# Kernel optimization log

Measured on AMD Instinct MI355X. Metric: run time of the kernel, lower is better.

## Reference

```python
import jax, jax.numpy as jnp
import numpy as np
from jax import lax

D = 1024          # channel / embedding dim
K = 2048          # codebook size
BN_EPS = 1e-5


def conv1d(x, w, b, stride):
    # x: [N, C, L], w: [O, I, k]
    y = lax.conv_general_dilated(x, w, window_strides=(stride,), padding='VALID',
                                 dimension_numbers=('NCH', 'OIH', 'NCH'))
    return y + b[None, :, None]


def batchnorm1d(x, gamma, beta):
    # training-mode BN: batch statistics over (N, L) per channel, biased variance
    mean = jnp.mean(x, axis=(0, 2), keepdims=True)
    var = jnp.var(x, axis=(0, 2), keepdims=True)
    return (x - mean) * lax.rsqrt(var + BN_EPS) * gamma[None, :, None] + beta[None, :, None]


def setup_inputs() -> dict:
    key = jax.random.key(0)
    ks = jax.random.split(key, 8)
    x = jax.random.normal(ks[0], (32, D, 1024), dtype=jnp.float32)
    conv1_w = jax.random.normal(ks[1], (D, D, 4), dtype=jnp.float32) * 0.02
    conv1_b = jnp.zeros((D,), dtype=jnp.float32)
    bn1_g = jnp.ones((D,), dtype=jnp.float32)
    bn1_b = jnp.zeros((D,), dtype=jnp.float32)
    conv2_w = jax.random.normal(ks[2], (D, D, 1), dtype=jnp.float32) * 0.02
    conv2_b = jnp.zeros((D,), dtype=jnp.float32)
    bn2_g = jnp.ones((D,), dtype=jnp.float32)
    bn2_b = jnp.zeros((D,), dtype=jnp.float32)
    codebook = jax.random.normal(ks[3], (K, D), dtype=jnp.float32)
    return {'x': x, 'conv1_w': conv1_w, 'conv1_b': conv1_b,
            'bn1_g': bn1_g, 'bn1_b': bn1_b,
            'conv2_w': conv2_w, 'conv2_b': conv2_b,
            'bn2_g': bn2_g, 'bn2_b': bn2_b,
            'codebook': codebook}


def encoder(x, conv1_w, conv1_b, bn1_g, bn1_b, conv2_w, conv2_b, bn2_g, bn2_b):
    h = conv1d(x, conv1_w, conv1_b, stride=2)           # [B, D, L']
    # ResidualWrapper(BN -> ReLU -> Conv1x1)
    r = batchnorm1d(h, bn1_g, bn1_b)
    r = jax.nn.relu(r)
    r = conv1d(r, conv2_w, conv2_b, stride=1)
    h = h + r
    h = batchnorm1d(h, bn2_g, bn2_b)
    return h


def vq(h, codebook):
    # axis=1 -> move channel axis last: [B, L', D]
    z = jnp.moveaxis(h, 1, -1)
    # squared Euclidean distances via ||z||^2 - 2 z.e + ||e||^2  (cdist+argmin)
    z2 = jnp.sum(z * z, axis=-1, keepdims=True)                  # [B, L', 1]
    e2 = jnp.sum(codebook * codebook, axis=-1)                   # [K]
    ze = jnp.einsum('bld,kd->blk', z, codebook)                  # [B, L', K]
    dist2 = z2 - 2.0 * ze + e2[None, None, :]
    ids = jnp.argmin(dist2, axis=-1)                             # [B, L'] int
    q = codebook[ids]                                            # [B, L', D]
    sg = lax.stop_gradient
    commitment = jnp.mean((z - sg(q)) ** 2)
    codebook_loss = jnp.mean((sg(z) - q) ** 2)
    # straight-through estimator
    q_st = z + sg(q - z)
    q_st = jnp.moveaxis(q_st, -1, 1)                             # back to [B, D, L']
    return q_st, ids, commitment, codebook_loss


def reference(x, conv1_w, conv1_b, bn1_g, bn1_b, conv2_w, conv2_b, bn2_g, bn2_b, codebook):
    h = encoder(x, conv1_w, conv1_b, bn1_g, bn1_b, conv2_w, conv2_b, bn2_g, bn2_b)
    q_st, ids, commitment, codebook_loss = vq(h, codebook)
    return q_st, ids, commitment, codebook_loss
```

## Files before the change

kernel.cpp:

```cpp
#include <hip/hip_runtime.h>
#include <hip/hip_bf16.h>
#include <cstdint>

#define DD 1024
#define LIN 1024
#define LP 511
#define LPAD 512
#define NBATCH 32
#define KCB 2048
#define BN_EPS 1e-5f

#define OUT_IDS 16744448u
#define OUT_LOSS 16760800u

#define WS_H1 0
#define WS_UNI 16777216
#define WS_XH  (WS_UNI)
#define WS_XL  (WS_UNI + 16777728)
#define WS_WTH (WS_UNI + 33555456)
#define WS_WTL (WS_UNI + 35652608)
#define WS_T2  (WS_UNI)
#define WS_RH  (WS_UNI + 16777216)
#define WS_RL  (WS_UNI + 25165824)
#define WS_ZH  WS_RH
#define WS_ZL  WS_RL
#define WS_W2H (WS_UNI + 33554432)
#define WS_W2L (WS_UNI + 34078720)
#define WS_CBH (WS_UNI + 34603008)
#define WS_CBL (WS_UNI + 35651584)
#define WS_AUX (WS_UNI + 37749760)
#define WS_A1 (WS_AUX + 0)
#define WS_B1 (WS_AUX + 1024)
#define WS_A2 (WS_AUX + 2048)
#define WS_B2 (WS_AUX + 3072)
#define WS_E2 (WS_AUX + 4096)
#define WS_SLOTS (WS_AUX + 6144)
#define WS_LOSS (WS_AUX + 6144 + 32704)

typedef __attribute__((ext_vector_type(8))) short bf16x8;
typedef __attribute__((ext_vector_type(4))) float f32x4;
typedef __attribute__((ext_vector_type(4))) unsigned short ushort4v;

__device__ __forceinline__ void async_cp16(const void* gsrc, void* ldst) {
  __builtin_amdgcn_global_load_lds(
      (const __attribute__((address_space(1))) unsigned int*)gsrc,
      (__attribute__((address_space(3))) unsigned int*)ldst, 16, 0, 0);
}

__device__ __forceinline__ void bf16split(float v, unsigned short& hi, unsigned short& lo) {
  __hip_bfloat16 h = __float2bfloat16(v);
  float hf = __bfloat162float(h);
  __hip_bfloat16 l = __float2bfloat16(v - hf);
  hi = *(unsigned short*)&h;
  lo = *(unsigned short*)&l;
}

__device__ inline float blockReduce256(float v, float* sb) {
#pragma unroll
  for (int off = 32; off > 0; off >>= 1) v += __shfl_down(v, off);
  __syncthreads();
  if ((threadIdx.x & 63) == 0) sb[threadIdx.x >> 6] = v;
  __syncthreads();
  return sb[0] + sb[1] + sb[2] + sb[3];
}

__device__ __forceinline__ void mfma_tiles_k(
    const unsigned short* __restrict__ srcw, unsigned short* sm, int lane,
    int wid, int nkc, int mrow, int nrow, int ko, f32x4 (&acc)[4][4]) {
  const unsigned short* As = sm;
  const unsigned short* Als = sm + 4096;
  const unsigned short* Bs = sm + 8192;
  const unsigned short* Bls = sm + 12288;
  for (int kc = 0; kc < nkc; ++kc) {
    const unsigned short* lanesrc =
        srcw + (size_t)kc * 32 + (size_t)(lane >> 2) * 1024 + (lane & 3) * 8;
    char* ldsbase = (char*)sm + wid * 8192;
#pragma unroll
    for (int q = 0; q < 8; ++q)
      async_cp16(lanesrc + (size_t)q * 16 * 1024, ldsbase + q * 1024);
    __syncthreads();
    bf16x8 fbh[4], fbl[4];
#pragma unroll
    for (int nt = 0; nt < 4; ++nt) {
      int r = nrow + nt * 16;
      fbh[nt] = *(const bf16x8*)(Bs + r * 32 + ko);
      fbl[nt] = *(const bf16x8*)(Bls + r * 32 + ko);
    }
#pragma unroll
    for (int mt = 0; mt < 4; ++mt) {
      int r = mrow + mt * 16;
      bf16x8 fah = *(const bf16x8*)(As + r * 32 + ko);
      bf16x8 fal = *(const bf16x8*)(Als + r * 32 + ko);
#pragma unroll
      for (int nt = 0; nt < 4; ++nt) {
        acc[mt][nt] = __builtin_amdgcn_mfma_f32_16x16x32_bf16(fah, fbh[nt], acc[mt][nt], 0, 0, 0);
        acc[mt][nt] = __builtin_amdgcn_mfma_f32_16x16x32_bf16(fah, fbl[nt], acc[mt][nt], 0, 0, 0);
        acc[mt][nt] = __builtin_amdgcn_mfma_f32_16x16x32_bf16(fal, fbh[nt], acc[mt][nt], 0, 0, 0);
      }
    }
    __syncthreads();
  }
}

__global__ __launch_bounds__(256) void split_w1_kernel(
    const float* __restrict__ w, unsigned short* __restrict__ wth,
    unsigned short* __restrict__ wtl) {
  int idx = blockIdx.x * 256 + threadIdx.x;
  int o = idx >> 10, i = idx & 1023;
  float4 v = *(const float4*)&w[(size_t)idx * 4];
  float vv[4] = {v.x, v.y, v.z, v.w};
#pragma unroll
  for (int t = 0; t < 4; ++t) {
    unsigned short hi, lo;
    bf16split(vv[t], hi, lo);
    size_t off = (((size_t)(t << 10) + o) << 10) + i;
    wth[off] = hi;
    wtl[off] = lo;
  }
}

__global__ __launch_bounds__(256) void split_rows_kernel(
    const float* __restrict__ src, unsigned short* __restrict__ dsth,
    unsigned short* __restrict__ dstl) {
  size_t base = ((size_t)blockIdx.x * 256 + threadIdx.x) * 4;
  float4 v = *(const float4*)&src[base];
  float vv[4] = {v.x, v.y, v.z, v.w};
  ushort4v h, l;
#pragma unroll
  for (int j = 0; j < 4; ++j) {
    unsigned short hi, lo;
    bf16split(vv[j], hi, lo);
    h[j] = hi;
    l[j] = lo;
  }
  *(ushort4v*)&dsth[base] = h;
  *(ushort4v*)&dstl[base] = l;
}

__global__ __launch_bounds__(256) void split_x_kernel(
    const float* __restrict__ x, unsigned short* __restrict__ xh,
    unsigned short* __restrict__ xl) {
  __shared__ float lsT[128 * 65];
  const int l0 = blockIdx.x * 128;
  const int i0 = blockIdx.y * 64;
  const int nB = blockIdx.z;
  const int tid = threadIdx.x;
#pragma unroll
  for (int p = 0; p < 8; ++p) {
    int flat = p * 256 + tid;
    int row = flat >> 5, col4 = (flat & 31) * 4;
    float4 v = *(const float4*)&x[((size_t)nB * DD + i0 + row) * LIN + l0 + col4];
    lsT[(col4 + 0) * 65 + row] = v.x;
    lsT[(col4 + 1) * 65 + row] = v.y;
    lsT[(col4 + 2) * 65 + row] = v.z;
    lsT[(col4 + 3) * 65 + row] = v.w;
  }
  __syncthreads();
  const int lo2 = (l0 >> 1);
#pragma unroll
  for (int p = 0; p < 16; ++p) {
    int cp = p * 4 + (tid >> 6);
    int il = tid & 63;
    float vE = lsT[(2 * cp) * 65 + il];
    float vO = lsT[(2 * cp + 1) * 65 + il];
    unsigned short hE, lE, hO, lO;
    bf16split(vE, hE, lE);
    bf16split(vO, hO, lO);
    size_t dE = (((size_t)(0 * 32 + nB) * 512) + lo2 + cp) * 1024 + i0 + il;
    size_t dO = (((size_t)(1 * 32 + nB) * 512) + lo2 + cp) * 1024 + i0 + il;
    xh[dE] = hE; xl[dE] = lE;
    xh[dO] = hO; xl[dO] = lO;
  }
}

__global__ __launch_bounds__(256) void trans_affine_split_kernel(
    const float* __restrict__ src, const float* __restrict__ a,
    const float* __restrict__ b, unsigned short* __restrict__ dsth,
    unsigned short* __restrict__ dstl, int do_relu) {
  __shared__ float lsT[128 * 65];
  const int l0 = blockIdx.x * 128;
  const int i0 = blockIdx.y * 64;
  const int nB = blockIdx.z;
  const int tid = threadIdx.x;
#pragma unroll
  for (int p = 0; p < 8; ++p) {
    int flat = p * 256 + tid;
    int row = flat >> 5, col4 = (flat & 31) * 4;
    float4 v = *(const float4*)&src[((size_t)nB * DD + i0 + row) * LPAD + l0 + col4];
    lsT[(col4 + 0) * 65 + row] = v.x;
    lsT[(col4 + 1) * 65 + row] = v.y;
    lsT[(col4 + 2) * 65 + row] = v.z;
    lsT[(col4 + 3) * 65 + row] = v.w;
  }
  __syncthreads();
  const int il = tid & 63;
  const float ac = a[i0 + il], bc = b[i0 + il];
#pragma unroll
  for (int p = 0; p < 32; ++p) {
    int cp = p * 4 + (tid >> 6);
    float v = fmaf(ac, lsT[cp * 65 + il], bc);
    if (do_relu) v = fmaxf(v, 0.f);
    unsigned short hi, lo;
    bf16split(v, hi, lo);
    size_t d = (((size_t)nB * 512) + l0 + cp) * 1024 + i0 + il;
    dsth[d] = hi;
    dstl[d] = lo;
  }
}

__global__ __launch_bounds__(256) void conv1_mfma_kernel(
    const unsigned short* __restrict__ wth, const unsigned short* __restrict__ wtl,
    const unsigned short* __restrict__ xh, const unsigned short* __restrict__ xl,
    const float* __restrict__ bias, float* __restrict__ h1) {
  __shared__ unsigned short sm[16384];
  const int tid = threadIdx.x;
  const int wid = tid >> 6, lane = tid & 63;
  const int lb = blockIdx.x * 128, ob = blockIdx.y * 128, nB = blockIdx.z;

  f32x4 acc[4][4];
#pragma unroll
  for (int a = 0; a < 4; ++a)
#pragma unroll
    for (int b = 0; b < 4; ++b) acc[a][b] = (f32x4){0.f, 0.f, 0.f, 0.f};

  const int wm = wid & 1, wn = wid >> 1;
  const int mrow = (wm << 6) + (lane & 15);
  const int nrow = (wn << 6) + (lane & 15);
  const int ko = (lane >> 4) << 3;

  for (int t = 0; t < 4; ++t) {
    const unsigned short* srcw;
    if (wid == 0)
      srcw = wth + (((size_t)(t << 10) + ob) << 10);
    else if (wid == 1)
      srcw = wtl + (((size_t)(t << 10) + ob) << 10);
    else {
      const unsigned short* xp = (wid == 2) ? xh : xl;
      srcw = xp + ((((size_t)((t & 1) * 32 + nB) * 512) + lb + (t >> 1)) << 10);
    }
    mfma_tiles_k(srcw, sm, lane, wid, 32, mrow, nrow, ko, acc);
  }

#pragma unroll
  for (int mt = 0; mt < 4; ++mt) {
    const int o_base = ob + (wm << 6) + mt * 16 + ((lane >> 4) << 2);
#pragma unroll
    for (int nt = 0; nt < 4; ++nt) {
      const int l = lb + (wn << 6) + nt * 16 + (lane & 15);
      if (l < LP) {
#pragma unroll
        for (int rg = 0; rg < 4; ++rg)
          h1[((size_t)(nB << 10) + o_base + rg) * LPAD + l] =
              acc[mt][nt][rg] + bias[o_base + rg];
      }
    }
  }
}

__global__ __launch_bounds__(256) void conv2_mfma_kernel(
    const unsigned short* __restrict__ w2h, const unsigned short* __restrict__ w2l,
    const unsigned short* __restrict__ rh, const unsigned short* __restrict__ rl,
    const float* __restrict__ b2c, const float* __restrict__ h1,
    float* __restrict__ t2) {
  __shared__ unsigned short sm[16384];
  const int tid = threadIdx.x;
  const int wid = tid >> 6, lane = tid & 63;
  const int lb = blockIdx.x * 128, ob = blockIdx.y * 128, nB = blockIdx.z;

  f32x4 acc[4][4];
#pragma unroll
  for (int a = 0; a < 4; ++a)
#pragma unroll
    for (int b = 0; b < 4; ++b) acc[a][b] = (f32x4){0.f, 0.f, 0.f, 0.f};

  const int wm = wid & 1, wn = wid >> 1;
  const int mrow = (wm << 6) + (lane & 15);
  const int nrow = (wn << 6) + (lane & 15);
  const int ko = (lane >> 4) << 3;

  const unsigned short* srcw =
      (wid == 0) ? w2h + ((size_t)ob << 10)
    : (wid == 1) ? w2l + ((size_t)ob << 10)
    : (wid == 2) ? rh + (((size_t)nB * 512 + lb) << 10)
                 : rl + (((size_t)nB * 512 + lb) << 10);
  mfma_tiles_k(srcw, sm, lane, wid, 32, mrow, nrow, ko, acc);

#pragma unroll
  for (int mt = 0; mt < 4; ++mt) {
    const int o_base = ob + (wm << 6) + mt * 16 + ((lane >> 4) << 2);
#pragma unroll
    for (int nt = 0; nt < 4; ++nt) {
      const int l = lb + (wn << 6) + nt * 16 + (lane & 15);
      if (l < LP) {
#pragma unroll
        for (int rg = 0; rg < 4; ++rg) {
          size_t off = ((size_t)(nB << 10) + o_base + rg) * LPAD + l;
          t2[off] = h1[off] + acc[mt][nt][rg] + b2c[o_base + rg];
        }
      }
    }
  }
}

__global__ __launch_bounds__(256) void dist_mfma_kernel(
    const unsigned short* __restrict__ cbh, const unsigned short* __restrict__ cbl,
    const unsigned short* __restrict__ zh, const unsigned short* __restrict__ zl,
    const float* __restrict__ e2, unsigned long long* __restrict__ slots) {
  __shared__ unsigned short sm[16384];
  __shared__ unsigned long long best[128];
  const int tid = threadIdx.x;
  const int wid = tid >> 6, lane = tid & 63;
  const int lb = blockIdx.x * 128, kb = blockIdx.y * 128, nB = blockIdx.z;

  f32x4 acc[4][4];
#pragma unroll
  for (int a = 0; a < 4; ++a)
#pragma unroll
    for (int b = 0; b < 4; ++b) acc[a][b] = (f32x4){0.f, 0.f, 0.f, 0.f};

  const int wm = wid & 1, wn = wid >> 1;
  const int mrow = (wm << 6) + (lane & 15);
  const int nrow = (wn << 6) + (lane & 15);
  const int ko = (lane >> 4) << 3;

  const unsigned short* srcw =
      (wid == 0) ? cbh + ((size_t)kb << 10)
    : (wid == 1) ? cbl + ((size_t)kb << 10)
    : (wid == 2) ? zh + (((size_t)nB * 512 + lb) << 10)
                 : zl + (((size_t)nB * 512 + lb) << 10);
  mfma_tiles_k(srcw, sm, lane, wid, 32, mrow, nrow, ko, acc);

  if (tid < 128) best[tid] = ~0ULL;
  __syncthreads();
#pragma unroll
  for (int nt = 0; nt < 4; ++nt) {
    const int col = (wn << 6) + nt * 16 + (lane & 15);
    float dmin = 3.4e38f;
    int kmin = 0;
#pragma unroll
    for (int mt = 0; mt < 4; ++mt) {
      const int kbase = kb + (wm << 6) + mt * 16 + ((lane >> 4) << 2);
#pragma unroll
      for (int rg = 0; rg < 4; ++rg) {
        float dist = fmaf(-2.f, acc[mt][nt][rg], e2[kbase + rg]);
        if (dist < dmin) { dmin = dist; kmin = kbase + rg; }
      }
    }
    unsigned long long pk =
        ((unsigned long long)__float_as_uint(dmin) << 32) | (unsigned)kmin;
    atomicMin(&best[col], pk);
  }
  __syncthreads();
  if (tid < 128) {
    int l = lb + tid;
    if (l < LP) atomicMin(&slots[(size_t)nB * LP + l], best[tid]);
  }
}

__global__ __launch_bounds__(256) void bn_stats_kernel(
    const float* __restrict__ src, const float* __restrict__ gamma,
    const float* __restrict__ beta, float* __restrict__ a_out,
    float* __restrict__ b_out) {
  __shared__ float sb[4];
  const int c = blockIdx.x;
  const float* p = src + (size_t)c * LPAD;
  float s1 = 0.f, s2 = 0.f;
  for (int idx = threadIdx.x; idx < NBATCH * LP; idx += 256) {
    int nn = idx / LP;
    int l = idx - nn * LP;
    float v = p[(size_t)nn * DD * LPAD + l];
    s1 += v;
    s2 = fmaf(v, v, s2);
  }
  s1 = blockReduce256(s1, sb);
  s2 = blockReduce256(s2, sb);
  if (threadIdx.x == 0) {
    const float inv = 1.f / (float)(NBATCH * LP);
    float m = s1 * inv;
    float var = fmaf(-m, m, s2 * inv);
    float a = gamma[c] * rsqrtf(var + BN_EPS);
    a_out[c] = a;
    b_out[c] = fmaf(-m, a, beta[c]);
  }
}

__global__ __launch_bounds__(256) void e2_kernel(const float* __restrict__ cb,
                                                 float* __restrict__ e2) {
  __shared__ float sb[4];
  const int k = blockIdx.x;
  float s = 0.f;
  for (int d = threadIdx.x; d < DD; d += 256) {
    float v = cb[(size_t)k * DD + d];
    s = fmaf(v, v, s);
  }
  s = blockReduce256(s, sb);
  if (threadIdx.x == 0) e2[k] = s;
}

__global__ __launch_bounds__(256) void gather_kernel(
    const float* __restrict__ t2, const float* __restrict__ cb,
    const float* __restrict__ a2, const float* __restrict__ b2,
    const unsigned long long* __restrict__ slots, float* __restrict__ out,
    float* __restrict__ loss_acc) {
  __shared__ int ks[64];
  __shared__ float sb[4];
  const int l0 = blockIdx.x * 64;
  const int n = blockIdx.y;
  const int tid = threadIdx.x, tx = tid & 63, ty = tid >> 6;
  if (tid < 64) {
    int l = l0 + tid;
    int k = 0;
    if (l < LP) {
      k = (int)(unsigned)(slots[(size_t)n * LP + l] & 0xffffffffULL);
      out[OUT_IDS + (size_t)n * LP + l] = (float)k;
    }
    ks[tid] = k;
  }
  __syncthreads();
  const int l = l0 + tx;
  const bool valid = (l < LP);
  const int k = ks[tx];
  const float* cbk = cb + (size_t)k * DD;
  const float* tn = t2 + (size_t)n * DD * LPAD;
  float* qo = out + (size_t)n * DD * LP;
  float lsum = 0.f;
  for (int d0 = 0; d0 < DD; d0 += 4) {
    const int d = d0 + ty;
    float q = cbk[d];
    if (valid) {
      float z = fmaf(a2[d], tn[(size_t)d * LPAD + l], b2[d]);
      qo[(size_t)d * LP + l] = q;
      float e = z - q;
      lsum = fmaf(e, e, lsum);
    }
  }
  lsum = blockReduce256(lsum, sb);
  if (tid == 0) atomicAdd(loss_acc, lsum);
}

__global__ void finalize_kernel(const float* __restrict__ loss_acc,
                                float* __restrict__ out) {
  if (threadIdx.x == 0) {
    float m = loss_acc[0] * (1.f / 16744448.f);
    out[OUT_LOSS] = m;
    out[OUT_LOSS + 1] = m;
  }
}

extern "C" void kernel_launch(void* const* d_in, const int* in_sizes, int n_in,
                              void* d_out, int out_size, void* d_ws,
                              size_t ws_size, hipStream_t stream) {
  const float* x = (const float*)d_in[0];
  const float* w1 = (const float*)d_in[1];
  const float* b1c = (const float*)d_in[2];
  const float* g1 = (const float*)d_in[3];
  const float* be1 = (const float*)d_in[4];
  const float* w2 = (const float*)d_in[5];
  const float* b2c = (const float*)d_in[6];
  const float* g2 = (const float*)d_in[7];
  const float* be2 = (const float*)d_in[8];
  const float* cb = (const float*)d_in[9];
  float* out = (float*)d_out;
  float* ws = (float*)d_ws;

  float* h1 = ws + WS_H1;
  float* t2 = ws + WS_T2;
  unsigned short* xh = (unsigned short*)(ws + WS_XH);
  unsigned short* xl = (unsigned short*)(ws + WS_XL);
  unsigned short* wth = (unsigned short*)(ws + WS_WTH);
  unsigned short* wtl = (unsigned short*)(ws + WS_WTL);
  unsigned short* rh = (unsigned short*)(ws + WS_RH);
  unsigned short* rl = (unsigned short*)(ws + WS_RL);
  unsigned short* zh = (unsigned short*)(ws + WS_ZH);
  unsigned short* zl = (unsigned short*)(ws + WS_ZL);
  unsigned short* w2h = (unsigned short*)(ws + WS_W2H);
  unsigned short* w2l = (unsigned short*)(ws + WS_W2L);
  unsigned short* cbh = (unsigned short*)(ws + WS_CBH);
  unsigned short* cbl = (unsigned short*)(ws + WS_CBL);
  float* a1 = ws + WS_A1;
  float* bb1 = ws + WS_B1;
  float* a2 = ws + WS_A2;
  float* bb2 = ws + WS_B2;
  float* e2 = ws + WS_E2;
  unsigned long long* slots = (unsigned long long*)(ws + WS_SLOTS);
  float* loss = ws + WS_LOSS;

  (void)hipMemsetAsync(slots, 0xFF,
                       (size_t)NBATCH * LP * sizeof(unsigned long long), stream);
  (void)hipMemsetAsync(loss, 0, sizeof(float), stream);

  split_w1_kernel<<<4096, 256, 0, stream>>>(w1, wth, wtl);
  split_x_kernel<<<dim3(8, 16, NBATCH), 256, 0, stream>>>(x, xh, xl);
  conv1_mfma_kernel<<<dim3(4, 8, NBATCH), 256, 0, stream>>>(wth, wtl, xh, xl,
                                                            b1c, h1);
  bn_stats_kernel<<<DD, 256, 0, stream>>>(h1, g1, be1, a1, bb1);
  split_rows_kernel<<<1024, 256, 0, stream>>>(w2, w2h, w2l);
  split_rows_kernel<<<2048, 256, 0, stream>>>(cb, cbh, cbl);
  e2_kernel<<<KCB, 256, 0, stream>>>(cb, e2);
  trans_affine_split_kernel<<<dim3(4, 16, NBATCH), 256, 0, stream>>>(
      h1, a1, bb1, rh, rl, 1);
  conv2_mfma_kernel<<<dim3(4, 8, NBATCH), 256, 0, stream>>>(w2h, w2l, rh, rl,
                                                            b2c, h1, t2);
  bn_stats_kernel<<<DD, 256, 0, stream>>>(t2, g2, be2, a2, bb2);
  trans_affine_split_kernel<<<dim3(4, 16, NBATCH), 256, 0, stream>>>(
      t2, a2, bb2, zh, zl, 0);
  dist_mfma_kernel<<<dim3(4, 16, NBATCH), 256, 0, stream>>>(cbh, cbl, zh, zl,
                                                            e2, slots);
  gather_kernel<<<dim3(8, NBATCH), 256, 0, stream>>>(t2, cb, a2, bb2, slots, out, loss);
  finalize_kernel<<<1, 64, 0, stream>>>(loss, out);
}
```

Baseline: 1.182 ms.

## Use 256x256 double-buffered swizzled MFMA tiles for conv and distance GEMMs

Replaces the 128x128, 4-wave GEMM core with a shared 256x256, 8-wave core used by conv1, conv2 and the distance kernels. The core double-buffers LDS in 128 KB of dynamic shared memory and prefetches the next K chunk with async copies while MFMAs run. It uses fine-grained vmcnt waits and barriers, an XOR swizzle against LDS bank conflicts, and setprio around the MFMA bursts. Larger tiles raise operand reuse and cut global traffic and barrier stalls. The cost is much higher register and LDS use per block, which limits occupancy to one block per CU and halves the grid size.

After: 1.025 ms. 13.3% less time.

```diff
diff --git a/kernel.cpp b/kernel.cpp
--- a/kernel.cpp
+++ b/kernel.cpp
@@ -64,41 +64,96 @@
   return sb[0] + sb[1] + sb[2] + sb[3];
 }
 
-__device__ __forceinline__ void mfma_tiles_k(
-    const unsigned short* __restrict__ srcw, unsigned short* sm, int lane,
-    int wid, int nkc, int mrow, int nrow, int ko, f32x4 (&acc)[4][4]) {
-  const unsigned short* As = sm;
-  const unsigned short* Als = sm + 4096;
-  const unsigned short* Bs = sm + 8192;
-  const unsigned short* Bls = sm + 12288;
-  for (int kc = 0; kc < nkc; ++kc) {
-    const unsigned short* lanesrc =
-        srcw + (size_t)kc * 32 + (size_t)(lane >> 2) * 1024 + (lane & 3) * 8;
-    char* ldsbase = (char*)sm + wid * 8192;
-#pragma unroll
-    for (int q = 0; q < 8; ++q)
-      async_cp16(lanesrc + (size_t)q * 16 * 1024, ldsbase + q * 1024);
-    __syncthreads();
-    bf16x8 fbh[4], fbl[4];
-#pragma unroll
-    for (int nt = 0; nt < 4; ++nt) {
-      int r = nrow + nt * 16;
-      fbh[nt] = *(const bf16x8*)(Bs + r * 32 + ko);
-      fbl[nt] = *(const bf16x8*)(Bls + r * 32 + ko);
+#define VMCNT(n) asm volatile("s_waitcnt vmcnt(" #n ")" ::: "memory")
+
+template <typename SF>
+__device__ __forceinline__ void stage_slot(const SF& sf, int c, int slot,
+                                           unsigned short* smbase, int wid,
+                                           int lane) {
+  int plane, r0;
+  if (slot < 4) {
+    plane = 2 + (slot >> 1);
+    r0 = ((slot & 1) << 7) + (wid << 4);
+  } else {
+    plane = wid & 1;
+    r0 = (((wid >> 1) & 1) << 7) + ((slot - 4) << 5) + ((wid >> 2) << 4);
+  }
+  const unsigned short* g = sf(c, plane) + (size_t)(r0 + (lane >> 2)) * 1024 +
+                            (((lane & 3) ^ ((lane >> 3) & 3)) << 3);
+  unsigned short* d = smbase + plane * 8192 + r0 * 32;
+  async_cp16(g, d);
+}
+
+template <typename SF>
+__device__ __forceinline__ void mfma256_core(const SF& sf, unsigned short* sm,
+                                             int nkc, f32x4 (&acc)[8][4]) {
+  const int tid = threadIdx.x;
+  const int wid = tid >> 6, lane = tid & 63;
+  const int wm = wid >> 2, wn = wid & 3;
+  const int slot16 = (((lane >> 4) ^ ((lane >> 1) & 3)) << 3);
+  const int arow = (wm << 7) + (lane & 15);
+  const int brow = (wn << 6) + (lane & 15);
+
+#pragma unroll
+  for (int s = 0; s < 8; ++s) stage_slot(sf, 0, s, sm, wid, lane);
+
+  bf16x8 fbh[4], fbl[4];
+  for (int c = 0; c < nkc; ++c) {
+    unsigned short* buf = sm + ((c & 1) << 15);
+    unsigned short* nbuf = sm + (((c + 1) & 1) << 15);
+    const unsigned short* As = buf;
+    const unsigned short* Als = buf + 8192;
+    const unsigned short* Bs = buf + 16384;
+    const unsigned short* Bls = buf + 24576;
+    const bool pre = (c + 1 < nkc);
+#pragma unroll
+    for (int p = 0; p < 4; ++p) {
+      if (pre) {
+        if (p == 0) { VMCNT(3); } else if (p == 1) { VMCNT(4); }
+        else if (p == 2) { VMCNT(5); } else { VMCNT(6); }
+      } else {
+        if (p == 0) { VMCNT(3); } else if (p == 1) { VMCNT(2); }
+        else if (p == 2) { VMCNT(1); } else { VMCNT(0); }
+      }
+      __builtin_amdgcn_s_barrier();
+      asm volatile("" ::: "memory");
+      __builtin_amdgcn_sched_barrier(0);
+      if (p == 0) {
+#pragma unroll
+        for (int nt = 0; nt < 4; ++nt) {
+          int r = brow + nt * 16;
+          fbh[nt] = *(const bf16x8*)(Bs + r * 32 + slot16);
+          fbl[nt] = *(const bf16x8*)(Bls + r * 32 + slot16);
+        }
+      }
+      bf16x8 fah0, fal0, fah1, fal1;
+      {
+        int r0 = arow + ((2 * p) << 4);
+        int r1 = r0 + 16;
+        fah0 = *(const bf16x8*)(As + r0 * 32 + slot16);
+        fal0 = *(const bf16x8*)(Als + r0 * 32 + slot16);
+        fah1 = *(const bf16x8*)(As + r1 * 32 + slot16);
+        fal1 = *(const bf16x8*)(Als + r1 * 32 + slot16);
+      }
+      if (pre) {
+        stage_slot(sf, c + 1, 2 * p + 0, nbuf, wid, lane);
+        stage_slot(sf, c + 1, 2 * p + 1, nbuf, wid, lane);
+      }
+      __builtin_amdgcn_s_setprio(1);
+#pragma unroll
+      for (int nt = 0; nt < 4; ++nt) {
+        acc[2 * p][nt] = __builtin_amdgcn_mfma_f32_16x16x32_bf16(fah0, fbh[nt], acc[2 * p][nt], 0, 0, 0);
+        acc[2 * p][nt] = __builtin_amdgcn_mfma_f32_16x16x32_bf16(fah0, fbl[nt], acc[2 * p][nt], 0, 0, 0);
+        acc[2 * p][nt] = __builtin_amdgcn_mfma_f32_16x16x32_bf16(fal0, fbh[nt], acc[2 * p][nt], 0, 0, 0);
+      }
+#pragma unroll
+      for (int nt = 0; nt < 4; ++nt) {
+        acc[2 * p + 1][nt] = __builtin_amdgcn_mfma_f32_16x16x32_bf16(fah1, fbh[nt], acc[2 * p + 1][nt], 0, 0, 0);
+        acc[2 * p + 1][nt] = __builtin_amdgcn_mfma_f32_16x16x32_bf16(fah1, fbl[nt], acc[2 * p + 1][nt], 0, 0, 0);
+        acc[2 * p + 1][nt] = __builtin_amdgcn_mfma_f32_16x16x32_bf16(fal1, fbh[nt], acc[2 * p + 1][nt], 0, 0, 0);
+      }
+      __builtin_amdgcn_s_setprio(0);
     }
-#pragma unroll
-    for (int mt = 0; mt < 4; ++mt) {
-      int r = mrow + mt * 16;
-      bf16x8 fah = *(const bf16x8*)(As + r * 32 + ko);
-      bf16x8 fal = *(const bf16x8*)(Als + r * 32 + ko);
-#pragma unroll
-      for (int nt = 0; nt < 4; ++nt) {
-        acc[mt][nt] = __builtin_amdgcn_mfma_f32_16x16x32_bf16(fah, fbh[nt], acc[mt][nt], 0, 0, 0);
-        acc[mt][nt] = __builtin_amdgcn_mfma_f32_16x16x32_bf16(fah, fbl[nt], acc[mt][nt], 0, 0, 0);
-        acc[mt][nt] = __builtin_amdgcn_mfma_f32_16x16x32_bf16(fal, fbh[nt], acc[mt][nt], 0, 0, 0);
-      }
-    }
-    __syncthreads();
   }
 }
 
@@ -208,42 +263,34 @@
   }
 }
 
-__global__ __launch_bounds__(256) void conv1_mfma_kernel(
+__global__ __launch_bounds__(512, 2) void conv1_mfma_kernel(
     const unsigned short* __restrict__ wth, const unsigned short* __restrict__ wtl,
     const unsigned short* __restrict__ xh, const unsigned short* __restrict__ xl,
     const float* __restrict__ bias, float* __restrict__ h1) {
-  __shared__ unsigned short sm[16384];
+  extern __shared__ unsigned short sm[];
   const int tid = threadIdx.x;
   const int wid = tid >> 6, lane = tid & 63;
-  const int lb = blockIdx.x * 128, ob = blockIdx.y * 128, nB = blockIdx.z;
-
-  f32x4 acc[4][4];
-#pragma unroll
-  for (int a = 0; a < 4; ++a)
+  const int lb = blockIdx.x * 256, ob = blockIdx.y * 256, nB = blockIdx.z;
+
+  f32x4 acc[8][4];
+#pragma unroll
+  for (int a = 0; a < 8; ++a)
 #pragma unroll
     for (int b = 0; b < 4; ++b) acc[a][b] = (f32x4){0.f, 0.f, 0.f, 0.f};
 
-  const int wm = wid & 1, wn = wid >> 1;
-  const int mrow = (wm << 6) + (lane & 15);
-  const int nrow = (wn << 6) + (lane & 15);
-  const int ko = (lane >> 4) << 3;
-
-  for (int t = 0; t < 4; ++t) {
-    const unsigned short* srcw;
-    if (wid == 0)
-      srcw = wth + (((size_t)(t << 10) + ob) << 10);
-    else if (wid == 1)
-      srcw = wtl + (((size_t)(t << 10) + ob) << 10);
-    else {
-      const unsigned short* xp = (wid == 2) ? xh : xl;
-      srcw = xp + ((((size_t)((t & 1) * 32 + nB) * 512) + lb + (t >> 1)) << 10);
-    }
-    mfma_tiles_k(srcw, sm, lane, wid, 32, mrow, nrow, ko, acc);
-  }
-
-#pragma unroll
-  for (int mt = 0; mt < 4; ++mt) {
-    const int o_base = ob + (wm << 6) + mt * 16 + ((lane >> 4) << 2);
+  auto sf = [&](int c, int plane) -> const unsigned short* {
+    int t = c >> 5, kc = c & 31;
+    if (plane == 0) return wth + ((((size_t)t << 10) + ob) << 10) + kc * 32;
+    if (plane == 1) return wtl + ((((size_t)t << 10) + ob) << 10) + kc * 32;
+    const unsigned short* xp = (plane == 2) ? xh : xl;
+    return xp + ((((size_t)((t & 1) * 32 + nB) * 512) + lb + (t >> 1)) << 10) + kc * 32;
+  };
+  mfma256_core(sf, sm, 128, acc);
+
+  const int wm = wid >> 2, wn = wid & 3;
+#pragma unroll
+  for (int mt = 0; mt < 8; ++mt) {
+    const int o_base = ob + (wm << 7) + mt * 16 + ((lane >> 4) << 2);
 #pragma unroll
     for (int nt = 0; nt < 4; ++nt) {
       const int l = lb + (wn << 6) + nt * 16 + (lane & 15);
@@ -257,37 +304,34 @@
   }
 }
 
-__global__ __launch_bounds__(256) void conv2_mfma_kernel(
+__global__ __launch_bounds__(512, 2) void conv2_mfma_kernel(
     const unsigned short* __restrict__ w2h, const unsigned short* __restrict__ w2l,
     const unsigned short* __restrict__ rh, const unsigned short* __restrict__ rl,
     const float* __restrict__ b2c, const float* __restrict__ h1,
     float* __restrict__ t2) {
-  __shared__ unsigned short sm[16384];
+  extern __shared__ unsigned short sm[];
   const int tid = threadIdx.x;
   const int wid = tid >> 6, lane = tid & 63;
-  const int lb = blockIdx.x * 128, ob = blockIdx.y * 128, nB = blockIdx.z;
-
-  f32x4 acc[4][4];
-#pragma unroll
-  for (int a = 0; a < 4; ++a)
+  const int lb = blockIdx.x * 256, ob = blockIdx.y * 256, nB = blockIdx.z;
+
+  f32x4 acc[8][4];
+#pragma unroll
+  for (int a = 0; a < 8; ++a)
 #pragma unroll
     for (int b = 0; b < 4; ++b) acc[a][b] = (f32x4){0.f, 0.f, 0.f, 0.f};
 
-  const int wm = wid & 1, wn = wid >> 1;
-  const int mrow = (wm << 6) + (lane & 15);
-  const int nrow = (wn << 6) + (lane & 15);
-  const int ko = (lane >> 4) << 3;
-
-  const unsigned short* srcw =
-      (wid == 0) ? w2h + ((size_t)ob << 10)
-    : (wid == 1) ? w2l + ((size_t)ob << 10)
-    : (wid == 2) ? rh + (((size_t)nB * 512 + lb) << 10)
-                 : rl + (((size_t)nB * 512 + lb) << 10);
-  mfma_tiles_k(srcw, sm, lane, wid, 32, mrow, nrow, ko, acc);
-
-#pragma unroll
-  for (int mt = 0; mt < 4; ++mt) {
-    const int o_base = ob + (wm << 6) + mt * 16 + ((lane >> 4) << 2);
+  auto sf = [&](int c, int plane) -> const unsigned short* {
+    if (plane == 0) return w2h + ((size_t)ob << 10) + (size_t)c * 32;
+    if (plane == 1) return w2l + ((size_t)ob << 10) + (size_t)c * 32;
+    const unsigned short* rp = (plane == 2) ? rh : rl;
+    return rp + (((size_t)nB * 512 + lb) << 10) + (size_t)c * 32;
+  };
+  mfma256_core(sf, sm, 32, acc);
+
+  const int wm = wid >> 2, wn = wid & 3;
+#pragma unroll
+  for (int mt = 0; mt < 8; ++mt) {
+    const int o_base = ob + (wm << 7) + mt * 16 + ((lane >> 4) << 2);
 #pragma unroll
     for (int nt = 0; nt < 4; ++nt) {
       const int l = lb + (wn << 6) + nt * 16 + (lane & 15);
@@ -302,44 +346,41 @@
   }
 }
 
-__global__ __launch_bounds__(256) void dist_mfma_kernel(
+__global__ __launch_bounds__(512, 2) void dist_mfma_kernel(
     const unsigned short* __restrict__ cbh, const unsigned short* __restrict__ cbl,
     const unsigned short* __restrict__ zh, const unsigned short* __restrict__ zl,
     const float* __restrict__ e2, unsigned long long* __restrict__ slots) {
-  __shared__ unsigned short sm[16384];
-  __shared__ unsigned long long best[128];
+  extern __shared__ unsigned short sm[];
+  unsigned long long* best = (unsigned long long*)(sm + 65536);
   const int tid = threadIdx.x;
   const int wid = tid >> 6, lane = tid & 63;
-  const int lb = blockIdx.x * 128, kb = blockIdx.y * 128, nB = blockIdx.z;
-
-  f32x4 acc[4][4];
-#pragma unroll
-  for (int a = 0; a < 4; ++a)
+  const int lb = blockIdx.x * 256, kb = blockIdx.y * 256, nB = blockIdx.z;
+
+  if (tid < 256) best[tid] = ~0ULL;
+
+  f32x4 acc[8][4];
+#pragma unroll
+  for (int a = 0; a < 8; ++a)
 #pragma unroll
     for (int b = 0; b < 4; ++b) acc[a][b] = (f32x4){0.f, 0.f, 0.f, 0.f};
 
-  const int wm = wid & 1, wn = wid >> 1;
-  const int mrow = (wm << 6) + (lane & 15);
-  const int nrow = (wn << 6) + (lane & 15);
-  const int ko = (lane >> 4) << 3;
-
-  const unsigned short* srcw =
-      (wid == 0) ? cbh + ((size_t)kb << 10)
-    : (wid == 1) ? cbl + ((size_t)kb << 10)
-    : (wid == 2) ? zh + (((size_t)nB * 512 + lb) << 10)
-                 : zl + (((size_t)nB * 512 + lb) << 10);
-  mfma_tiles_k(srcw, sm, lane, wid, 32, mrow, nrow, ko, acc);
-
-  if (tid < 128) best[tid] = ~0ULL;
-  __syncthreads();
+  auto sf = [&](int c, int plane) -> const unsigned short* {
+    if (plane == 0) return cbh + ((size_t)kb << 10) + (size_t)c * 32;
+    if (plane == 1) return cbl + ((size_t)kb << 10) + (size_t)c * 32;
+    const unsigned short* zp = (plane == 2) ? zh : zl;
+    return zp + (((size_t)nB * 512 + lb) << 10) + (size_t)c * 32;
+  };
+  mfma256_core(sf, sm, 32, acc);
+
+  const int wm = wid >> 2, wn = wid & 3;
 #pragma unroll
   for (int nt = 0; nt < 4; ++nt) {
     const int col = (wn << 6) + nt * 16 + (lane & 15);
     float dmin = 3.4e38f;
     int kmin = 0;
 #pragma unroll
-    for (int mt = 0; mt < 4; ++mt) {
-      const int kbase = kb + (wm << 6) + mt * 16 + ((lane >> 4) << 2);
+    for (int mt = 0; mt < 8; ++mt) {
+      const int kbase = kb + (wm << 7) + mt * 16 + ((lane >> 4) << 2);
 #pragma unroll
       for (int rg = 0; rg < 4; ++rg) {
         float dist = fmaf(-2.f, acc[mt][nt][rg], e2[kbase + rg]);
@@ -351,7 +392,7 @@
     atomicMin(&best[col], pk);
   }
   __syncthreads();
-  if (tid < 128) {
+  if (tid < 256) {
     int l = lb + tid;
     if (l < LP) atomicMin(&slots[(size_t)nB * LP + l], best[tid]);
   }
@@ -485,27 +526,38 @@
   unsigned long long* slots = (unsigned long long*)(ws + WS_SLOTS);
   float* loss = ws + WS_LOSS;
 
+  static int attr_done = 0;
+  if (!attr_done) {
+    (void)hipFuncSetAttribute(reinterpret_cast<const void*>(conv1_mfma_kernel),
+                              hipFuncAttributeMaxDynamicSharedMemorySize, 135168);
+    (void)hipFuncSetAttribute(reinterpret_cast<const void*>(conv2_mfma_kernel),
+                              hipFuncAttributeMaxDynamicSharedMemorySize, 135168);
+    (void)hipFuncSetAttribute(reinterpret_cast<const void*>(dist_mfma_kernel),
+                              hipFuncAttributeMaxDynamicSharedMemorySize, 135168);
+    attr_done = 1;
+  }
+
   (void)hipMemsetAsync(slots, 0xFF,
                        (size_t)NBATCH * LP * sizeof(unsigned long long), stream);
   (void)hipMemsetAsync(loss, 0, sizeof(float), stream);
 
   split_w1_kernel<<<4096, 256, 0, stream>>>(w1, wth, wtl);
   split_x_kernel<<<dim3(8, 16, NBATCH), 256, 0, stream>>>(x, xh, xl);
-  conv1_mfma_kernel<<<dim3(4, 8, NBATCH), 256, 0, stream>>>(wth, wtl, xh, xl,
-                                                            b1c, h1);
+  conv1_mfma_kernel<<<dim3(2, 4, NBATCH), 512, 131072, stream>>>(wth, wtl, xh,
+                                                                 xl, b1c, h1);
   bn_stats_kernel<<<DD, 256, 0, stream>>>(h1, g1, be1, a1, bb1);
   split_rows_kernel<<<1024, 256, 0, stream>>>(w2, w2h, w2l);
   split_rows_kernel<<<2048, 256, 0, stream>>>(cb, cbh, cbl);
   e2_kernel<<<KCB, 256, 0, stream>>>(cb, e2);
   trans_affine_split_kernel<<<dim3(4, 16, NBATCH), 256, 0, stream>>>(
       h1, a1, bb1, rh, rl, 1);
-  conv2_mfma_kernel<<<dim3(4, 8, NBATCH), 256, 0, stream>>>(w2h, w2l, rh, rl,
-                                                            b2c, h1, t2);
+  conv2_mfma_kernel<<<dim3(2, 4, NBATCH), 512, 131072, stream>>>(w2h, w2l, rh,
+                                                                 rl, b2c, h1, t2);
   bn_stats_kernel<<<DD, 256, 0, stream>>>(t2, g2, be2, a2, bb2);
   trans_affine_split_kernel<<<dim3(4, 16, NBATCH), 256, 0, stream>>>(
       t2, a2, bb2, zh, zl, 0);
-  dist_mfma_kernel<<<dim3(4, 16, NBATCH), 256, 0, stream>>>(cbh, cbl, zh, zl,
-                                                            e2, slots);
+  dist_mfma_kernel<<<dim3(2, 8, NBATCH), 512, 133120, stream>>>(cbh, cbl, zh,
+                                                                zl, e2, slots);
   gather_kernel<<<dim3(8, NBATCH), 256, 0, stream>>>(t2, cb, a2, bb2, slots, out, loss);
   finalize_kernel<<<1, 64, 0, stream>>>(loss, out);
 }
```
